# Kernel optimization log

Hardware: AMD Instinct MI355X
Metric: run time of the kernel (lower is better)

The kernel has to match this reference:

```python
import jax, jax.numpy as jnp
import numpy as np

IN_CH = 512
MID = max(IN_CH // 8, 1)


def setup_inputs() -> dict:
    key = jax.random.key(0)
    ks = jax.random.split(key, 8)
    B, C, H, W = 4, IN_CH, 64, 64
    s = 0.05
    x = jax.random.normal(ks[0], (B, C, H, W), dtype=jnp.float32)
    wq = jax.random.normal(ks[1], (MID, C), dtype=jnp.float32) * s
    bq = jnp.zeros((MID,), dtype=jnp.float32)
    wk = jax.random.normal(ks[2], (MID, C), dtype=jnp.float32) * s
    bk = jnp.zeros((MID,), dtype=jnp.float32)
    wv = jax.random.normal(ks[3], (C, C), dtype=jnp.float32) * s
    bv = jnp.zeros((C,), dtype=jnp.float32)
    alpha = jnp.ones((1,), dtype=jnp.float32) * 0.5  # nonzero so attention path is exercised
    return {"x": x, "wq": wq, "bq": bq, "wk": wk, "bk": bk, "wv": wv, "bv": bv, "alpha": alpha}


def reference(x, wq, bq, wk, bk, wv, bv, alpha):
    B, C, H, W = x.shape
    N = H * W
    xf = x.reshape(B, C, N)  # [B, C, N]
    # 1x1 convs == per-position channel GEMMs
    q = jnp.einsum('mc,bcn->bnm', wq, xf) + bq  # [B, N, mid]
    k = jnp.einsum('mc,bcn->bmn', wk, xf) + bk[None, :, None]  # [B, mid, N]
    v = jnp.einsum('dc,bcn->bdn', wv, xf) + bv[None, :, None]  # [B, C, N]
    attn = jax.nn.softmax(jnp.einsum('bnm,bmk->bnk', q, k), axis=-1)  # [B, N, N]
    out = jnp.einsum('bdn,bkn->bdk', v, attn)  # v @ attn^T -> [B, C, N]
    out = out.reshape(B, C, H, W)
    return alpha * out + x
```

## Files before the change

### kernel.cpp

```cpp
#include <hip/hip_runtime.h>

#define BB 4
#define CD 512
#define NP 4096
#define MID 64
#define PSTR 88

typedef _Float16 half8 __attribute__((ext_vector_type(8)));
typedef _Float16 half4 __attribute__((ext_vector_type(4)));
typedef float floatx4 __attribute__((ext_vector_type(4)));

#define LOG2E 1.4426950408889634f

__global__ __launch_bounds__(256) void prep_w(
    const float* __restrict__ wq, const float* __restrict__ wk,
    const float* __restrict__ wv, const float* __restrict__ bq,
    const float* __restrict__ bk, const float* __restrict__ bv,
    _Float16* __restrict__ w_h, float* __restrict__ bias) {
  int idx = blockIdx.x * 256 + threadIdx.x;
  for (int i = idx; i < 640 * 512; i += gridDim.x * 256) {
    int r = i >> 9, c = i & 511;
    float v = (r < 64) ? wq[(r << 9) + c] * LOG2E
            : (r < 128) ? wk[((r - 64) << 9) + c]
                        : wv[((r - 128) << 9) + c];
    w_h[i] = (_Float16)v;
  }
  if (idx < 640) {
    float v = (idx < 64) ? bq[idx] * LOG2E
            : (idx < 128) ? bk[idx - 64]
                          : bv[idx - 128];
    bias[idx] = v;
  }
}

__global__ __launch_bounds__(256) void transpose_x(const float* __restrict__ x,
                                                   _Float16* __restrict__ xt) {
  __shared__ float tile[64][65];
  int b = blockIdx.z, c0 = blockIdx.y * 64, n0 = blockIdx.x * 64;
  int t = threadIdx.x;
  const float* xb = x + (size_t)b * CD * NP;
#pragma unroll
  for (int k = 0; k < 16; k++) {
    int cl = k * 4 + (t >> 6);
    int nl = t & 63;
    tile[cl][nl] = xb[(size_t)(c0 + cl) * NP + n0 + nl];
  }
  __syncthreads();
  _Float16* xtb = xt + ((size_t)b * NP + n0) * CD + c0;
#pragma unroll
  for (int k = 0; k < 2; k++) {
    int nl = k * 32 + (t >> 3);
    int cl = (t & 7) * 8;
    half8 pk;
#pragma unroll
    for (int i = 0; i < 8; i++) pk[i] = (_Float16)tile[cl + i][nl];
    *(half8*)(xtb + (size_t)nl * CD + cl) = pk;
  }
}

__global__ __launch_bounds__(256, 2) void proj_qkv(
    const _Float16* __restrict__ w_h, const float* __restrict__ bias,
    const _Float16* __restrict__ xt, _Float16* __restrict__ q_h,
    _Float16* __restrict__ k_h, _Float16* __restrict__ v_h) {
  __shared__ _Float16 xls[64 * 512];
  int t = threadIdx.x, w = t >> 6, lane = t & 63;
  int col = lane & 15, quad = lane >> 4;
  int rbh = blockIdx.x, nb = blockIdx.y, b = blockIdx.z;
  int n0 = nb * 64;
  const _Float16* xtb = xt + ((size_t)b * NP + n0) * CD;

#pragma unroll
  for (int j = 0; j < 16; j++) {
    int u = t + j * 256;
    int row = u >> 6, un = u & 63;
    *(half8*)(xls + row * 512 + ((un ^ (row & 7)) << 3)) =
        *(const half8*)(xtb + (size_t)row * CD + un * 8);
  }
  __syncthreads();

  int rw = rbh * 320 + w * 80;
  floatx4 acc[5][4] = {};
  for (int c = 0; c < CD; c += 32) {
    int cu = c >> 3;
    half8 a[5], bf[4];
#pragma unroll
    for (int i = 0; i < 5; i++)
      a[i] = *(const half8*)(w_h + (size_t)(rw + i * 16 + col) * CD + c + quad * 8);
#pragma unroll
    for (int j = 0; j < 4; j++) {
      int row = j * 16 + col;
      bf[j] = *(const half8*)(xls + row * 512 + (((cu + quad) ^ (row & 7)) << 3));
    }
#pragma unroll
    for (int i = 0; i < 5; i++)
#pragma unroll
      for (int j = 0; j < 4; j++)
        acc[i][j] = __builtin_amdgcn_mfma_f32_16x16x32_f16(a[i], bf[j], acc[i][j], 0, 0, 0);
  }

#pragma unroll
  for (int i = 0; i < 5; i++) {
    int r0 = rw + i * 16;
    float bi[4];
#pragma unroll
    for (int rr = 0; rr < 4; rr++) bi[rr] = bias[r0 + quad * 4 + rr];
    if (r0 < 128) {
      _Float16* dst = (r0 < 64 ? q_h + (size_t)b * NP * MID + r0
                               : k_h + (size_t)b * NP * MID + (r0 - 64));
#pragma unroll
      for (int j = 0; j < 4; j++) {
        int n = n0 + j * 16 + col;
        half4 pk;
#pragma unroll
        for (int rr = 0; rr < 4; rr++) pk[rr] = (_Float16)(acc[i][j][rr] + bi[rr]);
        *(half4*)(dst + (size_t)n * MID + quad * 4) = pk;
      }
    } else {
      int dbase = r0 - 128 + quad * 4;
#pragma unroll
      for (int j = 0; j < 4; j++) {
        int n = n0 + j * 16 + col;
#pragma unroll
        for (int rr = 0; rr < 4; rr++)
          v_h[((size_t)b * CD + dbase + rr) * NP + n] =
              (_Float16)(acc[i][j][rr] + bi[rr]);
      }
    }
  }
}

__global__ __launch_bounds__(256) void rowmax(const _Float16* __restrict__ q_h,
                                              const _Float16* __restrict__ k_h,
                                              float* __restrict__ M) {
  int qb = blockIdx.x, b = blockIdx.y;
  int t = threadIdx.x, w = t >> 6, lane = t & 63;
  int col = lane & 15, quad = lane >> 4;
  int q0 = qb * 32;
  const _Float16* qp = q_h + ((size_t)b * NP + q0) * MID;
  half8 bq[2][2];
#pragma unroll
  for (int qt = 0; qt < 2; qt++)
#pragma unroll
    for (int h = 0; h < 2; h++)
      bq[qt][h] = *(const half8*)(qp + (size_t)(qt * 16 + col) * MID + h * 32 + quad * 8);
  const _Float16* kp = k_h + ((size_t)b * NP + (size_t)w * 1024) * MID;
  float m[2] = {-1e30f, -1e30f};
#pragma unroll 4
  for (int n = 0; n < 1024; n += 16) {
    half8 ak0 = *(const half8*)(kp + (size_t)(n + col) * MID + quad * 8);
    half8 ak1 = *(const half8*)(kp + (size_t)(n + col) * MID + 32 + quad * 8);
#pragma unroll
    for (int qt = 0; qt < 2; qt++) {
      floatx4 s = {};
      s = __builtin_amdgcn_mfma_f32_16x16x32_f16(ak0, bq[qt][0], s, 0, 0, 0);
      s = __builtin_amdgcn_mfma_f32_16x16x32_f16(ak1, bq[qt][1], s, 0, 0, 0);
      m[qt] = fmaxf(m[qt], fmaxf(fmaxf(s[0], s[1]), fmaxf(s[2], s[3])));
    }
  }
  __shared__ float red[4][2][16];
#pragma unroll
  for (int qt = 0; qt < 2; qt++) {
    m[qt] = fmaxf(m[qt], __shfl_xor(m[qt], 16));
    m[qt] = fmaxf(m[qt], __shfl_xor(m[qt], 32));
  }
  if (quad == 0) {
    red[w][0][col] = m[0];
    red[w][1][col] = m[1];
  }
  __syncthreads();
  if (t < 32) {
    int qt = t >> 4, c = t & 15;
    float mm = fmaxf(fmaxf(red[0][qt][c], red[1][qt][c]),
                     fmaxf(red[2][qt][c], red[3][qt][c]));
    M[(size_t)b * NP + q0 + t] = mm;
  }
}

__global__ __launch_bounds__(256, 2) void attn_pv(
    const _Float16* __restrict__ q_h, const _Float16* __restrict__ k_h,
    const _Float16* __restrict__ v_h, const float* __restrict__ M,
    const float* __restrict__ x, const float* __restrict__ alpha_p,
    float* __restrict__ out) {
  int bid = blockIdx.x;
  int combo = bid & 7;
  int b = combo >> 1, ds = combo & 1;
  int qb = bid >> 3;
  int q0 = qb * 64, d0 = ds * 256;

  int t = threadIdx.x, w = t >> 6, lane = t & 63;
  int col = lane & 15, quad = lane >> 4;

  __shared__ _Float16 pbuf[2][64 * PSTR];
  __shared__ float lred[4][4][16];
  __shared__ float lfin[64];

  const _Float16* qp = q_h + ((size_t)b * NP + q0) * MID;
  half8 bq[4][2];
#pragma unroll
  for (int qt = 0; qt < 4; qt++)
#pragma unroll
    for (int h = 0; h < 2; h++)
      bq[qt][h] = *(const half8*)(qp + (size_t)(qt * 16 + col) * MID + h * 32 + quad * 8);
  float Mq[4];
#pragma unroll
  for (int qt = 0; qt < 4; qt++) Mq[qt] = M[(size_t)b * NP + q0 + qt * 16 + col];

  const _Float16* kp = k_h + (size_t)b * NP * MID;
  const _Float16* vp = v_h + ((size_t)(b * CD + d0) + w * 64) * NP;

  floatx4 acc[4][4] = {};
  float lp[4] = {0.f, 0.f, 0.f, 0.f};

  for (int ci = 0; ci < 64; ci++) {
    int nc = ci * 64;
    _Float16* pb = pbuf[ci & 1];

    const _Float16* kr = kp + (size_t)(nc + w * 16 + col) * MID;
    half8 ak0 = *(const half8*)(kr + quad * 8);
    half8 ak1 = *(const half8*)(kr + 32 + quad * 8);

    half8 av[2][4];
#pragma unroll
    for (int f = 0; f < 2; f++)
#pragma unroll
      for (int dt = 0; dt < 4; dt++)
        av[f][dt] = *(const half8*)(vp + (size_t)(dt * 16 + col) * NP + nc + f * 32 + quad * 8);

#pragma unroll
    for (int qt = 0; qt < 4; qt++) {
      floatx4 s = {};
      s = __builtin_amdgcn_mfma_f32_16x16x32_f16(ak0, bq[qt][0], s, 0, 0, 0);
      s = __builtin_amdgcn_mfma_f32_16x16x32_f16(ak1, bq[qt][1], s, 0, 0, 0);
      half4 pk;
#pragma unroll
      for (int r = 0; r < 4; r++) {
        float p = exp2f(s[r] - Mq[qt]);
        lp[qt] += p;
        pk[r] = (_Float16)p;
      }
      *(half4*)(pb + (qt * 16 + col) * PSTR + w * 16 + quad * 4) = pk;
    }
    __syncthreads();

#pragma unroll
    for (int f = 0; f < 2; f++) {
      half8 bp[4];
#pragma unroll
      for (int qt = 0; qt < 4; qt++)
        bp[qt] = *(const half8*)(pb + (qt * 16 + col) * PSTR + f * 32 + quad * 8);
#pragma unroll
      for (int dt = 0; dt < 4; dt++)
#pragma unroll
        for (int qt = 0; qt < 4; qt++)
          acc[dt][qt] = __builtin_amdgcn_mfma_f32_16x16x32_f16(av[f][dt], bp[qt], acc[dt][qt], 0, 0, 0);
    }
  }

#pragma unroll
  for (int qt = 0; qt < 4; qt++) {
    lp[qt] += __shfl_xor(lp[qt], 16);
    lp[qt] += __shfl_xor(lp[qt], 32);
    if (quad == 0) lred[w][qt][col] = lp[qt];
  }
  __syncthreads();
  if (t < 64) {
    int qt = t >> 4, c = t & 15;
    float l = lred[0][qt][c] + lred[1][qt][c] + lred[2][qt][c] + lred[3][qt][c];
    lfin[t] = alpha_p[0] / l;
  }
  __syncthreads();

  const float* xp = x + ((size_t)(b * CD + d0) + w * 64) * NP;
  float* op = out + ((size_t)(b * CD + d0) + w * 64) * NP;
#pragma unroll
  for (int dt = 0; dt < 4; dt++)
#pragma unroll
    for (int qt = 0; qt < 4; qt++) {
      float linv = lfin[qt * 16 + col];
#pragma unroll
      for (int r = 0; r < 4; r++) {
        size_t o = (size_t)(dt * 16 + quad * 4 + r) * NP + q0 + qt * 16 + col;
        op[o] = acc[dt][qt][r] * linv + xp[o];
      }
    }
}

extern "C" void kernel_launch(void* const* d_in, const int* in_sizes, int n_in,
                              void* d_out, int out_size, void* d_ws, size_t ws_size,
                              hipStream_t stream) {
  const float* x     = (const float*)d_in[0];
  const float* wq    = (const float*)d_in[1];
  const float* bq    = (const float*)d_in[2];
  const float* wk    = (const float*)d_in[3];
  const float* bk    = (const float*)d_in[4];
  const float* wv    = (const float*)d_in[5];
  const float* bv    = (const float*)d_in[6];
  const float* alpha = (const float*)d_in[7];
  float* out = (float*)d_out;

  char* ws = (char*)d_ws;
  _Float16* w_h  = (_Float16*)(ws);
  float*    bias = (float*)(ws + 655360);
  float*    Mbuf = (float*)(ws + 657920);
  _Float16* xt   = (_Float16*)(ws + 723456);
  _Float16* q_h  = (_Float16*)(ws + 17500672);
  _Float16* k_h  = (_Float16*)(ws + 19597824);
  _Float16* v_h  = (_Float16*)(ws + 21694976);

  prep_w<<<1280, 256, 0, stream>>>(wq, wk, wv, bq, bk, bv, w_h, bias);
  transpose_x<<<dim3(64, 8, BB), 256, 0, stream>>>(x, xt);
  proj_qkv<<<dim3(2, 64, BB), 256, 0, stream>>>(w_h, bias, xt, q_h, k_h, v_h);
  rowmax<<<dim3(128, BB), 256, 0, stream>>>(q_h, k_h, Mbuf);
  attn_pv<<<512, 256, 0, stream>>>(q_h, k_h, v_h, Mbuf, x, alpha, out);
}
```

Baseline: 308.1 us.

## Software-pipeline K/V global loads one chunk ahead in attention loop

Prefetches the next chunk's K and V fragments into registers while computing the current chunk, so global load latency overlaps with the QK MFMAs, exp and PV MFMAs. It also swaps exp2f for the raw hardware exp2 builtin, replaces __syncthreads with an explicit lgkmcnt wait plus s_barrier, hoists all P loads before the MFMAs, and raises wave priority around the MFMA block. The cost is higher register pressure, which could reduce occupancy or cause spills. The last iteration also issues a redundant wrapped-around load.

Result: no change. 309.0 us (+0.3%).

```diff
diff --git a/kernel.cpp b/kernel.cpp
--- a/kernel.cpp
+++ b/kernel.cpp
@@ -205,26 +205,34 @@
 #pragma unroll
   for (int qt = 0; qt < 4; qt++) Mq[qt] = M[(size_t)b * NP + q0 + qt * 16 + col];
 
-  const _Float16* kp = k_h + (size_t)b * NP * MID;
+  const _Float16* kw = k_h + ((size_t)b * NP + w * 16 + col) * MID + quad * 8;
   const _Float16* vp = v_h + ((size_t)(b * CD + d0) + w * 64) * NP;
 
   floatx4 acc[4][4] = {};
   float lp[4] = {0.f, 0.f, 0.f, 0.f};
 
+  half8 ak0 = *(const half8*)(kw);
+  half8 ak1 = *(const half8*)(kw + 32);
+  half8 av[2][4];
+#pragma unroll
+  for (int f = 0; f < 2; f++)
+#pragma unroll
+    for (int dt = 0; dt < 4; dt++)
+      av[f][dt] = *(const half8*)(vp + (size_t)(dt * 16 + col) * NP + f * 32 + quad * 8);
+
+#pragma unroll 2
   for (int ci = 0; ci < 64; ci++) {
-    int nc = ci * 64;
     _Float16* pb = pbuf[ci & 1];
-
-    const _Float16* kr = kp + (size_t)(nc + w * 16 + col) * MID;
-    half8 ak0 = *(const half8*)(kr + quad * 8);
-    half8 ak1 = *(const half8*)(kr + 32 + quad * 8);
-
-    half8 av[2][4];
+    int ncn = ((ci + 1) & 63) * 64;
+
+    half8 an0 = *(const half8*)(kw + (size_t)ncn * MID);
+    half8 an1 = *(const half8*)(kw + (size_t)ncn * MID + 32);
+    half8 avn[2][4];
 #pragma unroll
     for (int f = 0; f < 2; f++)
 #pragma unroll
       for (int dt = 0; dt < 4; dt++)
-        av[f][dt] = *(const half8*)(vp + (size_t)(dt * 16 + col) * NP + nc + f * 32 + quad * 8);
+        avn[f][dt] = *(const half8*)(vp + (size_t)(dt * 16 + col) * NP + ncn + f * 32 + quad * 8);
 
 #pragma unroll
     for (int qt = 0; qt < 4; qt++) {
@@ -234,26 +242,38 @@
       half4 pk;
 #pragma unroll
       for (int r = 0; r < 4; r++) {
-        float p = exp2f(s[r] - Mq[qt]);
+        float p = __builtin_amdgcn_exp2f(s[r] - Mq[qt]);
         lp[qt] += p;
         pk[r] = (_Float16)p;
       }
       *(half4*)(pb + (qt * 16 + col) * PSTR + w * 16 + quad * 4) = pk;
     }
-    __syncthreads();
-
-#pragma unroll
-    for (int f = 0; f < 2; f++) {
-      half8 bp[4];
+
+    asm volatile("s_waitcnt lgkmcnt(0)" ::: "memory");
+    __builtin_amdgcn_s_barrier();
+
+    half8 bp[2][4];
+#pragma unroll
+    for (int f = 0; f < 2; f++)
 #pragma unroll
       for (int qt = 0; qt < 4; qt++)
-        bp[qt] = *(const half8*)(pb + (qt * 16 + col) * PSTR + f * 32 + quad * 8);
+        bp[f][qt] = *(const half8*)(pb + (qt * 16 + col) * PSTR + f * 32 + quad * 8);
+    __builtin_amdgcn_s_setprio(1);
+#pragma unroll
+    for (int f = 0; f < 2; f++)
 #pragma unroll
       for (int dt = 0; dt < 4; dt++)
 #pragma unroll
         for (int qt = 0; qt < 4; qt++)
-          acc[dt][qt] = __builtin_amdgcn_mfma_f32_16x16x32_f16(av[f][dt], bp[qt], acc[dt][qt], 0, 0, 0);
-    }
+          acc[dt][qt] = __builtin_amdgcn_mfma_f32_16x16x32_f16(av[f][dt], bp[f][qt], acc[dt][qt], 0, 0, 0);
+    __builtin_amdgcn_s_setprio(0);
+
+    ak0 = an0; ak1 = an1;
+#pragma unroll
+    for (int f = 0; f < 2; f++)
+#pragma unroll
+      for (int dt = 0; dt < 4; dt++)
+        av[f][dt] = avn[f][dt];
   }
 
 #pragma unroll
```

## Software-pipeline K/V global loads and swizzle P shared buffer in attn_pv

Applied to the files above, without the earlier changes.

Restructures the attn_pv main loop so the K and V fragments for the next chunk are loaded into a second register set while the current chunk is computed, using a manual ping-pong unroll with asm pins and sched barriers. The padded P shared buffer is replaced by an unpadded buffer with an XOR swizzle to avoid bank conflicts. It also uses the raw exp2 builtin, a lighter barrier and s_setprio around the PV MFMAs. The extra register set raises register pressure and may hurt occupancy. The last iteration prefetches a wrapped-around chunk that is never used.

After: 309.4 us. No clear change (+0.4%).

```diff
diff --git a/kernel.cpp b/kernel.cpp
--- a/kernel.cpp
+++ b/kernel.cpp
@@ -4,7 +4,6 @@
 #define CD 512
 #define NP 4096
 #define MID 64
-#define PSTR 88
 
 typedef _Float16 half8 __attribute__((ext_vector_type(8)));
 typedef _Float16 half4 __attribute__((ext_vector_type(4)));
@@ -189,8 +188,9 @@
 
   int t = threadIdx.x, w = t >> 6, lane = t & 63;
   int col = lane & 15, quad = lane >> 4;
-
-  __shared__ _Float16 pbuf[2][64 * PSTR];
+  int c7 = col & 7;
+
+  __shared__ _Float16 pbuf[2][64 * 64];
   __shared__ float lred[4][4][16];
   __shared__ float lfin[64];
 
@@ -205,56 +205,81 @@
 #pragma unroll
   for (int qt = 0; qt < 4; qt++) Mq[qt] = M[(size_t)b * NP + q0 + qt * 16 + col];
 
-  const _Float16* kp = k_h + (size_t)b * NP * MID;
+  const _Float16* kw = k_h + ((size_t)b * NP + w * 16 + col) * MID + quad * 8;
   const _Float16* vp = v_h + ((size_t)(b * CD + d0) + w * 64) * NP;
+
+  int wru = (((w * 2 + (quad >> 1)) ^ c7) << 3) + ((quad & 1) << 2);
+  int rdu0 = ((quad ^ c7) << 3);
+  int rdu1 = (((4 + quad) ^ c7) << 3);
 
   floatx4 acc[4][4] = {};
   float lp[4] = {0.f, 0.f, 0.f, 0.f};
 
-  for (int ci = 0; ci < 64; ci++) {
-    int nc = ci * 64;
-    _Float16* pb = pbuf[ci & 1];
-
-    const _Float16* kr = kp + (size_t)(nc + w * 16 + col) * MID;
-    half8 ak0 = *(const half8*)(kr + quad * 8);
-    half8 ak1 = *(const half8*)(kr + 32 + quad * 8);
-
-    half8 av[2][4];
-#pragma unroll
-    for (int f = 0; f < 2; f++)
-#pragma unroll
-      for (int dt = 0; dt < 4; dt++)
-        av[f][dt] = *(const half8*)(vp + (size_t)(dt * 16 + col) * NP + nc + f * 32 + quad * 8);
-
-#pragma unroll
-    for (int qt = 0; qt < 4; qt++) {
-      floatx4 s = {};
-      s = __builtin_amdgcn_mfma_f32_16x16x32_f16(ak0, bq[qt][0], s, 0, 0, 0);
-      s = __builtin_amdgcn_mfma_f32_16x16x32_f16(ak1, bq[qt][1], s, 0, 0, 0);
-      half4 pk;
-#pragma unroll
-      for (int r = 0; r < 4; r++) {
-        float p = exp2f(s[r] - Mq[qt]);
-        lp[qt] += p;
-        pk[r] = (_Float16)p;
-      }
-      *(half4*)(pb + (qt * 16 + col) * PSTR + w * 16 + quad * 4) = pk;
-    }
-    __syncthreads();
-
-#pragma unroll
-    for (int f = 0; f < 2; f++) {
-      half8 bp[4];
-#pragma unroll
-      for (int qt = 0; qt < 4; qt++)
-        bp[qt] = *(const half8*)(pb + (qt * 16 + col) * PSTR + f * 32 + quad * 8);
-#pragma unroll
-      for (int dt = 0; dt < 4; dt++)
-#pragma unroll
-        for (int qt = 0; qt < 4; qt++)
-          acc[dt][qt] = __builtin_amdgcn_mfma_f32_16x16x32_f16(av[f][dt], bp[qt], acc[dt][qt], 0, 0, 0);
-    }
-  }
+#define PIN10(K0, K1, AV)                                                      \
+  asm volatile("" : "+v"(K0), "+v"(K1), "+v"(AV[0][0]), "+v"(AV[0][1]),        \
+                    "+v"(AV[0][2]), "+v"(AV[0][3]), "+v"(AV[1][0]),            \
+                    "+v"(AV[1][1]), "+v"(AV[1][2]), "+v"(AV[1][3]))
+
+  half8 kA0, kA1, kB0, kB1;
+  half8 avA[2][4], avB[2][4];
+  kA0 = *(const half8*)(kw);
+  kA1 = *(const half8*)(kw + 32);
+#pragma unroll
+  for (int f = 0; f < 2; f++)
+#pragma unroll
+    for (int dt = 0; dt < 4; dt++)
+      avA[f][dt] = *(const half8*)(vp + (size_t)(dt * 16 + col) * NP + f * 32 + quad * 8);
+  PIN10(kA0, kA1, avA);
+
+#define CHUNK_BODY(K0, K1, AV, NK0, NK1, NAV, ci)                              \
+  {                                                                            \
+    int ncn_ = (((ci) + 1) & 63) * 64;                                         \
+    NK0 = *(const half8*)(kw + (size_t)ncn_ * MID);                            \
+    NK1 = *(const half8*)(kw + (size_t)ncn_ * MID + 32);                       \
+    _Pragma("unroll") for (int f_ = 0; f_ < 2; f_++)                           \
+      _Pragma("unroll") for (int dt_ = 0; dt_ < 4; dt_++)                      \
+        NAV[f_][dt_] = *(const half8*)(vp + (size_t)(dt_ * 16 + col) * NP +    \
+                                       ncn_ + f_ * 32 + quad * 8);             \
+    __builtin_amdgcn_sched_barrier(0);                                         \
+    _Float16* pb_ = pbuf[(ci) & 1];                                            \
+    _Pragma("unroll") for (int qt_ = 0; qt_ < 4; qt_++) {                      \
+      floatx4 s_ = {};                                                         \
+      s_ = __builtin_amdgcn_mfma_f32_16x16x32_f16(K0, bq[qt_][0], s_, 0, 0, 0);\
+      s_ = __builtin_amdgcn_mfma_f32_16x16x32_f16(K1, bq[qt_][1], s_, 0, 0, 0);\
+      half4 pk_;                                                               \
+      _Pragma("unroll") for (int r_ = 0; r_ < 4; r_++) {                       \
+        float p_ = __builtin_amdgcn_exp2f(s_[r_] - Mq[qt_]);                   \
+        lp[qt_] += p_;                                                         \
+        pk_[r_] = (_Float16)p_;                                                \
+      }                                                                        \
+      *(half4*)(pb_ + (qt_ * 16 + col) * 64 + wru) = pk_;                      \
+    }                                                                          \
+    asm volatile("s_waitcnt lgkmcnt(0)" ::: "memory");                         \
+    __builtin_amdgcn_s_barrier();                                              \
+    half8 bp0_[4], bp1_[4];                                                    \
+    _Pragma("unroll") for (int qt_ = 0; qt_ < 4; qt_++)                        \
+      bp0_[qt_] = *(const half8*)(pb_ + (qt_ * 16 + col) * 64 + rdu0);         \
+    _Pragma("unroll") for (int qt_ = 0; qt_ < 4; qt_++)                        \
+      bp1_[qt_] = *(const half8*)(pb_ + (qt_ * 16 + col) * 64 + rdu1);         \
+    __builtin_amdgcn_s_setprio(1);                                             \
+    _Pragma("unroll") for (int dt_ = 0; dt_ < 4; dt_++)                        \
+      _Pragma("unroll") for (int qt_ = 0; qt_ < 4; qt_++)                      \
+        acc[dt_][qt_] = __builtin_amdgcn_mfma_f32_16x16x32_f16(                \
+            AV[0][dt_], bp0_[qt_], acc[dt_][qt_], 0, 0, 0);                    \
+    _Pragma("unroll") for (int dt_ = 0; dt_ < 4; dt_++)                        \
+      _Pragma("unroll") for (int qt_ = 0; qt_ < 4; qt_++)                      \
+        acc[dt_][qt_] = __builtin_amdgcn_mfma_f32_16x16x32_f16(                \
+            AV[1][dt_], bp1_[qt_], acc[dt_][qt_], 0, 0, 0);                    \
+    __builtin_amdgcn_s_setprio(0);                                             \
+    PIN10(NK0, NK1, NAV);                                                      \
+  }
+
+  for (int ci = 0; ci < 64; ci += 2) {
+    CHUNK_BODY(kA0, kA1, avA, kB0, kB1, avB, ci);
+    CHUNK_BODY(kB0, kB1, avB, kA0, kA1, avA, ci + 1);
+  }
+#undef CHUNK_BODY
+#undef PIN10
 
 #pragma unroll
   for (int qt = 0; qt < 4; qt++) {
```

## Compute full P tile per wave and transpose via ds_bpermute, dropping LDS and barriers

Applied to the files above, without the earlier changes.

Each wave now computes QK scores for all 64 keys of the chunk itself instead of sharing P through a double-buffered LDS tile. It rearranges the fp16 probabilities into MFMA B-operand layout with ds_bpermute lane shuffles. This removes the per-iteration __syncthreads and the LDS round trip, and the row-sum reduction no longer crosses waves. The cost is 4x redundant QK MFMAs and exp2 per wave plus 16 bpermutes per q-tile, and it switches to the fast native exp2 intrinsic.

Result: slower. 392.4 us (+27.4%).

```diff
diff --git a/kernel.cpp b/kernel.cpp
--- a/kernel.cpp
+++ b/kernel.cpp
@@ -4,11 +4,12 @@
 #define CD 512
 #define NP 4096
 #define MID 64
-#define PSTR 88
 
 typedef _Float16 half8 __attribute__((ext_vector_type(8)));
 typedef _Float16 half4 __attribute__((ext_vector_type(4)));
 typedef float floatx4 __attribute__((ext_vector_type(4)));
+typedef unsigned int uint2v __attribute__((ext_vector_type(2)));
+typedef unsigned int uint4v __attribute__((ext_vector_type(4)));
 
 #define LOG2E 1.4426950408889634f
 
@@ -190,10 +191,6 @@
   int t = threadIdx.x, w = t >> 6, lane = t & 63;
   int col = lane & 15, quad = lane >> 4;
 
-  __shared__ _Float16 pbuf[2][64 * PSTR];
-  __shared__ float lred[4][4][16];
-  __shared__ float lfin[64];
-
   const _Float16* qp = q_h + ((size_t)b * NP + q0) * MID;
   half8 bq[4][2];
 #pragma unroll
@@ -207,68 +204,82 @@
 
   const _Float16* kp = k_h + (size_t)b * NP * MID;
   const _Float16* vp = v_h + ((size_t)(b * CD + d0) + w * 64) * NP;
+  float alpha = alpha_p[0];
 
   floatx4 acc[4][4] = {};
   float lp[4] = {0.f, 0.f, 0.f, 0.f};
 
+  int src_lo = (col + 16 * ((quad & 1) * 2)) << 2;
+  int src_hi = src_lo + (16 << 2);
+  int hiSel = quad & 2;
+
   for (int ci = 0; ci < 64; ci++) {
     int nc = ci * 64;
-    _Float16* pb = pbuf[ci & 1];
-
-    const _Float16* kr = kp + (size_t)(nc + w * 16 + col) * MID;
-    half8 ak0 = *(const half8*)(kr + quad * 8);
-    half8 ak1 = *(const half8*)(kr + 32 + quad * 8);
-
+
+    half8 ak[4][2];
+#pragma unroll
+    for (int kf = 0; kf < 4; kf++) {
+      const _Float16* kr = kp + (size_t)(nc + kf * 16 + col) * MID + quad * 8;
+      ak[kf][0] = *(const half8*)(kr);
+      ak[kf][1] = *(const half8*)(kr + 32);
+    }
     half8 av[2][4];
 #pragma unroll
-    for (int f = 0; f < 2; f++)
+    for (int kb = 0; kb < 2; kb++)
 #pragma unroll
       for (int dt = 0; dt < 4; dt++)
-        av[f][dt] = *(const half8*)(vp + (size_t)(dt * 16 + col) * NP + nc + f * 32 + quad * 8);
+        av[kb][dt] = *(const half8*)(vp + (size_t)(dt * 16 + col) * NP + nc + kb * 32 + quad * 8);
 
 #pragma unroll
     for (int qt = 0; qt < 4; qt++) {
-      floatx4 s = {};
-      s = __builtin_amdgcn_mfma_f32_16x16x32_f16(ak0, bq[qt][0], s, 0, 0, 0);
-      s = __builtin_amdgcn_mfma_f32_16x16x32_f16(ak1, bq[qt][1], s, 0, 0, 0);
-      half4 pk;
-#pragma unroll
-      for (int r = 0; r < 4; r++) {
-        float p = exp2f(s[r] - Mq[qt]);
-        lp[qt] += p;
-        pk[r] = (_Float16)p;
-      }
-      *(half4*)(pb + (qt * 16 + col) * PSTR + w * 16 + quad * 4) = pk;
-    }
-    __syncthreads();
-
-#pragma unroll
-    for (int f = 0; f < 2; f++) {
-      half8 bp[4];
-#pragma unroll
-      for (int qt = 0; qt < 4; qt++)
-        bp[qt] = *(const half8*)(pb + (qt * 16 + col) * PSTR + f * 32 + quad * 8);
-#pragma unroll
-      for (int dt = 0; dt < 4; dt++)
-#pragma unroll
-        for (int qt = 0; qt < 4; qt++)
-          acc[dt][qt] = __builtin_amdgcn_mfma_f32_16x16x32_f16(av[f][dt], bp[qt], acc[dt][qt], 0, 0, 0);
-    }
-  }
-
+      uint2v pw[4];
+#pragma unroll
+      for (int kf = 0; kf < 4; kf++) {
+        floatx4 s = {};
+        s = __builtin_amdgcn_mfma_f32_16x16x32_f16(ak[kf][0], bq[qt][0], s, 0, 0, 0);
+        s = __builtin_amdgcn_mfma_f32_16x16x32_f16(ak[kf][1], bq[qt][1], s, 0, 0, 0);
+        half4 pk;
+#pragma unroll
+        for (int r = 0; r < 4; r++) {
+          float p = __builtin_amdgcn_exp2f(s[r] - Mq[qt]);
+          lp[qt] += p;
+          pk[r] = (_Float16)p;
+        }
+        pw[kf] = __builtin_bit_cast(uint2v, pk);
+      }
+#pragma unroll
+      for (int kb = 0; kb < 2; kb++) {
+        unsigned int wv0, wv1, wv2, wv3;
+        {
+          int a0 = __builtin_amdgcn_ds_bpermute(src_lo, (int)pw[2 * kb][0]);
+          int b0 = __builtin_amdgcn_ds_bpermute(src_lo, (int)pw[2 * kb + 1][0]);
+          wv0 = hiSel ? b0 : a0;
+          int a1 = __builtin_amdgcn_ds_bpermute(src_lo, (int)pw[2 * kb][1]);
+          int b1 = __builtin_amdgcn_ds_bpermute(src_lo, (int)pw[2 * kb + 1][1]);
+          wv1 = hiSel ? b1 : a1;
+          int a2 = __builtin_amdgcn_ds_bpermute(src_hi, (int)pw[2 * kb][0]);
+          int b2 = __builtin_amdgcn_ds_bpermute(src_hi, (int)pw[2 * kb + 1][0]);
+          wv2 = hiSel ? b2 : a2;
+          int a3 = __builtin_amdgcn_ds_bpermute(src_hi, (int)pw[2 * kb][1]);
+          int b3 = __builtin_amdgcn_ds_bpermute(src_hi, (int)pw[2 * kb + 1][1]);
+          wv3 = hiSel ? b3 : a3;
+        }
+        uint4v wvv = {wv0, wv1, wv2, wv3};
+        half8 bp = __builtin_bit_cast(half8, wvv);
+#pragma unroll
+        for (int dt = 0; dt < 4; dt++)
+          acc[dt][qt] = __builtin_amdgcn_mfma_f32_16x16x32_f16(av[kb][dt], bp, acc[dt][qt], 0, 0, 0);
+      }
+    }
+  }
+
+  float linv[4];
 #pragma unroll
   for (int qt = 0; qt < 4; qt++) {
     lp[qt] += __shfl_xor(lp[qt], 16);
     lp[qt] += __shfl_xor(lp[qt], 32);
-    if (quad == 0) lred[w][qt][col] = lp[qt];
-  }
-  __syncthreads();
-  if (t < 64) {
-    int qt = t >> 4, c = t & 15;
-    float l = lred[0][qt][c] + lred[1][qt][c] + lred[2][qt][c] + lred[3][qt][c];
-    lfin[t] = alpha_p[0] / l;
-  }
-  __syncthreads();
+    linv[qt] = alpha / lp[qt];
+  }
 
   const float* xp = x + ((size_t)(b * CD + d0) + w * 64) * NP;
   float* op = out + ((size_t)(b * CD + d0) + w * 64) * NP;
@@ -276,11 +287,10 @@
   for (int dt = 0; dt < 4; dt++)
 #pragma unroll
     for (int qt = 0; qt < 4; qt++) {
-      float linv = lfin[qt * 16 + col];
 #pragma unroll
       for (int r = 0; r < 4; r++) {
         size_t o = (size_t)(dt * 16 + quad * 4 + r) * NP + q0 + qt * 16 + col;
-        op[o] = acc[dt][qt][r] * linv + xp[o];
+        op[o] = acc[dt][qt][r] * linv[qt] + xp[o];
       }
     }
 }
```
